# Optimization experiments

Hardware: AMD Instinct MI355X
Metric: run time of the kernel (lower is better)

## Reference

```python
import jax, jax.numpy as jnp
import numpy as np

B, S, D, H, G = 4, 2048, 1024, 16, 32
HD = D // H
LN_EPS = 1e-5


def _lin_init(key, fan_in, fan_out):
    kw, kb = jax.random.split(key)
    bound = 1.0 / np.sqrt(fan_in)
    W = jax.random.uniform(kw, (fan_in, fan_out), jnp.float32, -bound, bound)
    b = jax.random.uniform(kb, (fan_out,), jnp.float32, -bound, bound)
    return W, b


def setup_inputs() -> dict:
    key = jax.random.key(0)
    ks = jax.random.split(key, 9)
    x = jax.random.normal(ks[0], (B, S, D), jnp.float32)
    geo_features = jax.random.normal(ks[1], (B, G), jnp.float32)
    Wq, bq = _lin_init(ks[2], D, D)
    Wk, bk = _lin_init(ks[3], D, D)
    Wv, bv = _lin_init(ks[4], D, D)
    Wo, bo = _lin_init(ks[5], D, D)
    ge_W1, ge_b1 = _lin_init(ks[6], G, D)
    ln_g = jnp.ones((D,), jnp.float32)
    ln_b = jnp.zeros((D,), jnp.float32)
    ge_W2, ge_b2 = _lin_init(ks[7], D, D)
    gm_W, gm_b = _lin_init(ks[8], D, H)
    return dict(x=x, geo_features=geo_features, Wq=Wq, bq=bq, Wk=Wk, bk=bk,
                Wv=Wv, bv=bv, Wo=Wo, bo=bo, ge_W1=ge_W1, ge_b1=ge_b1,
                ln_g=ln_g, ln_b=ln_b, ge_W2=ge_W2, ge_b2=ge_b2,
                gm_W=gm_W, gm_b=gm_b)


def reference(x, geo_features, Wq, bq, Wk, bk, Wv, bv, Wo, bo,
              ge_W1, ge_b1, ln_g, ln_b, ge_W2, ge_b2, gm_W, gm_b):
    # QKV projections -> (B, H, S, HD)
    def split_heads(t):
        return t.reshape(B, S, H, HD).transpose(0, 2, 1, 3)
    Q = split_heads(x @ Wq + bq)
    K = split_heads(x @ Wk + bk)
    V = split_heads(x @ Wv + bv)

    # geo encoder: Linear -> LayerNorm -> ReLU -> Linear
    h = geo_features @ ge_W1 + ge_b1                      # (B, D)
    mu = jnp.mean(h, axis=-1, keepdims=True)
    var = jnp.mean(jnp.square(h - mu), axis=-1, keepdims=True)
    h = (h - mu) / jnp.sqrt(var + LN_EPS) * ln_g + ln_b
    h = jax.nn.relu(h)
    geo_encoded = h @ ge_W2 + ge_b2                       # (B, D)
    geo_mod = jax.nn.sigmoid(geo_encoded @ gm_W + gm_b)   # (B, H)

    scale = 1.0 / np.sqrt(HD)
    scores = jnp.einsum('bhqd,bhkd->bhqk', Q, K) * scale  # (B, H, S, S)
    scores = scores * (1.0 + geo_mod[:, :, None, None])
    attn = jax.nn.softmax(scores, axis=-1)                # dropout in eval mode: identity
    ctx = jnp.einsum('bhqk,bhkd->bhqd', attn, V)          # (B, H, S, HD)
    ctx = ctx.transpose(0, 2, 1, 3).reshape(B, S, D)
    out = ctx @ Wo + bo
    return out, attn
```

## Files before the change

### kernel.cpp

```cpp
#include <hip/hip_runtime.h>

typedef __attribute__((ext_vector_type(8))) short bf16x8;
typedef __attribute__((ext_vector_type(4))) float f32x4;
typedef __attribute__((ext_vector_type(4))) unsigned short us4;
typedef unsigned short u16;

#define MB (1024*1024)

#define WAITV(N) asm volatile("s_waitcnt vmcnt(" #N ")" ::: "memory")
#define WAITL0() asm volatile("s_waitcnt lgkmcnt(0)" ::: "memory")
#define BAR()    __builtin_amdgcn_s_barrier()
#define SCHEDB() __builtin_amdgcn_sched_barrier(0)

__device__ __forceinline__ u16 f2bf(float f) {
    unsigned u = __float_as_uint(f);
    unsigned r = (u + 0x7fffu + ((u >> 16) & 1u)) >> 16;
    return (u16)r;
}

__device__ __forceinline__ unsigned cvtpk(float a, float b) {
    unsigned r;
    asm("v_cvt_pk_bf16_f32 %0, %1, %2" : "=v"(r) : "v"(a), "v"(b));
    return r;
}

__device__ __forceinline__ f32x4 mfma16(bf16x8 a, bf16x8 b, f32x4 c) {
    return __builtin_amdgcn_mfma_f32_16x16x32_bf16(a, b, c, 0, 0, 0);
}

__device__ __forceinline__ void gload16(const void* g, void* l) {
    __builtin_amdgcn_global_load_lds(
        (__attribute__((address_space(1))) void*)(unsigned long long)g,
        (__attribute__((address_space(3))) void*)l, 16, 0, 0);
}

__global__ __launch_bounds__(256) void k_cvtx(const float* __restrict__ x, u16* __restrict__ xb) {
    const long long i = (long long)blockIdx.x * 256 + threadIdx.x;
    const float4* xp = (const float4*)x;
    float4 a = xp[i*2], b = xp[i*2+1];
    bf16x8 o;
    o[0]=(short)f2bf(a.x); o[1]=(short)f2bf(a.y); o[2]=(short)f2bf(a.z); o[3]=(short)f2bf(a.w);
    o[4]=(short)f2bf(b.x); o[5]=(short)f2bf(b.y); o[6]=(short)f2bf(b.z); o[7]=(short)f2bf(b.w);
    *(bf16x8*)&xb[i*8] = o;
}

__global__ __launch_bounds__(256) void k_wtcvt(const float* __restrict__ W0, const float* __restrict__ W1,
                                               const float* __restrict__ W2, const float* __restrict__ W3,
                                               u16* __restrict__ wt) {
    __shared__ float tl[32][33];
    const int t = threadIdx.x, z = blockIdx.z;
    const float* W = (z==0)?W0:(z==1)?W1:(z==2)?W2:W3;
    const int k0 = blockIdx.x*32, n0 = blockIdx.y*32;
    const int r = t >> 3, c4 = (t & 7) * 4;
    float4 v = *(const float4*)&W[(long long)(k0+r)*1024 + n0 + c4];
    tl[r][c4] = v.x; tl[r][c4+1] = v.y; tl[r][c4+2] = v.z; tl[r][c4+3] = v.w;
    __syncthreads();
    us4 ov;
    ov[0] = f2bf(tl[c4+0][r]); ov[1] = f2bf(tl[c4+1][r]);
    ov[2] = f2bf(tl[c4+2][r]); ov[3] = f2bf(tl[c4+3][r]);
    *(us4*)&wt[((long long)z << 20) + (long long)(n0+r)*1024 + k0 + c4] = ov;
}

__global__ __launch_bounds__(1024) void k_geo1(const float* __restrict__ geo, const float* __restrict__ W1,
                                               const float* __restrict__ b1, const float* __restrict__ lng,
                                               const float* __restrict__ lnb, float* __restrict__ hr) {
    const int b = blockIdx.x, j = threadIdx.x;
    float acc = b1[j];
    #pragma unroll 8
    for (int g = 0; g < 32; ++g) acc += geo[b*32+g] * W1[(long long)g*1024 + j];
    float s1 = acc, s2 = acc*acc;
    #pragma unroll
    for (int m = 1; m < 64; m <<= 1) { s1 += __shfl_xor(s1, m); s2 += __shfl_xor(s2, m); }
    __shared__ float r1[16], r2[16];
    __shared__ float mu_s, rv_s;
    const int wid = threadIdx.x >> 6, lid = threadIdx.x & 63;
    if (lid == 0) { r1[wid] = s1; r2[wid] = s2; }
    __syncthreads();
    if (threadIdx.x == 0) {
        float S1 = 0.f, S2 = 0.f;
        for (int i = 0; i < 16; ++i) { S1 += r1[i]; S2 += r2[i]; }
        float mu = S1 / 1024.f;
        float var = S2 / 1024.f - mu*mu;
        mu_s = mu; rv_s = rsqrtf(var + 1e-5f);
    }
    __syncthreads();
    float hv = (acc - mu_s) * rv_s * lng[j] + lnb[j];
    hr[b*1024 + j] = fmaxf(hv, 0.f);
}

__global__ __launch_bounds__(256) void k_geo2(const float* __restrict__ hr, const float* __restrict__ W2,
                                              const float* __restrict__ b2, float* __restrict__ ge) {
    const int b = blockIdx.x >> 2;
    const int j = (blockIdx.x & 3)*256 + threadIdx.x;
    __shared__ float hs[1024];
    #pragma unroll
    for (int i = 0; i < 4; ++i) hs[threadIdx.x*4 + i] = hr[b*1024 + threadIdx.x*4 + i];
    __syncthreads();
    float acc = b2[j];
    #pragma unroll 8
    for (int d = 0; d < 1024; ++d) acc += hs[d] * W2[(long long)d*1024 + j];
    ge[b*1024 + j] = acc;
}

__global__ __launch_bounds__(64) void k_geo3(const float* __restrict__ ge, const float* __restrict__ gmW,
                                             const float* __restrict__ gmb, float* __restrict__ qs) {
    const int t = threadIdx.x;
    const int b = t >> 4, hh = t & 15;
    float acc = gmb[hh];
    #pragma unroll 8
    for (int d = 0; d < 1024; ++d) acc += ge[b*1024 + d] * gmW[d*16 + hh];
    qs[t] = 0.125f * (1.f + 1.f/(1.f + __expf(-acc)));
}

__global__ __launch_bounds__(256) void k_qkv_gemm(const u16* __restrict__ xb, const u16* __restrict__ wtq,
                                                  const float* __restrict__ bq, const float* __restrict__ bk,
                                                  const float* __restrict__ bv, u16* __restrict__ outq) {
    __shared__ u16 lA[128*64];
    __shared__ u16 lB[128*64];
    const int t = threadIdx.x, z = blockIdx.z;
    const int m0 = blockIdx.y * 128, n0 = blockIdx.x * 128;
    const u16* wt = wtq + (long long)z * (1024*1024);
    const float* bias = (z==0) ? bq : (z==1) ? bk : bv;
    u16* out = outq + (long long)z * 8388608;
    const int w = t >> 6, l = t & 63, lm = l & 15, lg = l >> 4;
    const int wr = (w >> 1) * 64, wc = (w & 1) * 64;
    f32x4 acc[4][4] = {};
    const char* gA = (const char*)xb + (long long)(m0 + (t>>3))*2048 + (t&7)*16;
    const char* gB = (const char*)wt + (long long)(n0 + (t>>3))*2048 + (t&7)*16;
    char* lAp = (char*)lA + t*16;
    char* lBp = (char*)lB + t*16;
    for (int k0 = 0; k0 < 1024; k0 += 64) {
        #pragma unroll
        for (int i = 0; i < 4; ++i) {
            gload16(gA + (long long)i*32*2048, lAp + i*4096);
            gload16(gB + (long long)i*32*2048, lBp + i*4096);
        }
        gA += 128; gB += 128;
        __syncthreads();
        #pragma unroll
        for (int kk = 0; kk < 2; ++kk) {
            bf16x8 af[4], bfr[4];
            #pragma unroll
            for (int mi = 0; mi < 4; ++mi)
                af[mi] = *(const bf16x8*)((const char*)lA + (wr + mi*16 + lm)*128 + kk*64 + lg*16);
            #pragma unroll
            for (int ni = 0; ni < 4; ++ni)
                bfr[ni] = *(const bf16x8*)((const char*)lB + (wc + ni*16 + lm)*128 + kk*64 + lg*16);
            #pragma unroll
            for (int mi = 0; mi < 4; ++mi)
                #pragma unroll
                for (int ni = 0; ni < 4; ++ni)
                    acc[mi][ni] = mfma16(af[mi], bfr[ni], acc[mi][ni]);
        }
        __syncthreads();
    }
    #pragma unroll
    for (int ni = 0; ni < 4; ++ni) {
        const int n = n0 + wc + ni*16 + lm;
        const float bn = bias[n];
        const int hh = n >> 6, d = n & 63;
        #pragma unroll
        for (int mi = 0; mi < 4; ++mi) {
            #pragma unroll
            for (int r = 0; r < 4; ++r) {
                const int m = m0 + wr + mi*16 + lg*4 + r;
                const int b = m >> 11, s = m & 2047;
                out[(((long long)b*16 + hh)*2048 + s)*64 + d] = f2bf(acc[mi][ni][r] + bn);
            }
        }
    }
}

__global__ __launch_bounds__(256) void k_vtrans(const u16* __restrict__ vb, u16* __restrict__ vt) {
    __shared__ u16 tl[64][40];
    const int t = threadIdx.x;
    const int bh = blockIdx.z, s0 = blockIdx.y*64, d0 = blockIdx.x*32;
    const u16* vsrc = vb + (long long)bh*2048*64;
    {
        const int sl = t >> 2, dg = t & 3;
        bf16x8 v = *(const bf16x8*)&vsrc[(long long)(s0+sl)*64 + d0 + dg*8];
        *(bf16x8*)&tl[sl][dg*8] = v;
    }
    __syncthreads();
    {
        const int dl = t >> 3, sg = t & 7;
        bf16x8 o;
        #pragma unroll
        for (int j = 0; j < 8; ++j) o[j] = (short)tl[sg*8+j][dl];
        *(bf16x8*)&vt[((long long)bh*64 + d0+dl)*2048 + s0 + sg*8] = o;
    }
}

__global__ __launch_bounds__(512, 4) void k_attn(const u16* __restrict__ Qb, const u16* __restrict__ Kb,
                                                 const u16* __restrict__ Vt, const float* __restrict__ qsv,
                                                 float* __restrict__ attn_out, u16* __restrict__ ctxb) {
    __shared__ char lds[65536];

    const int nl = blockIdx.x;
    const int ob = (nl & 7)*64 + (nl >> 3);
    const int bh = ob >> 3, qt = ob & 7;
    const int t = threadIdx.x, w = t >> 6, l = t & 63, lm = l & 15, lg = l >> 4;
    const int q0 = qt * 256;
    const float qs = qsv[bh];

    const char* KB = (const char*)Kb + (long long)bh * 262144;
    const char* VB = (const char*)Vt + (long long)bh * 262144;

    bf16x8 qf[2][2];
    {
        const char* QB = (const char*)Qb + (long long)bh * 262144;
        #pragma unroll
        for (int ms = 0; ms < 2; ++ms)
            #pragma unroll
            for (int kc = 0; kc < 2; ++kc)
                qf[ms][kc] = *(const bf16x8*)(QB + (long long)(q0 + w*32 + ms*16 + lm)*128 + kc*64 + lg*16);
    }

    const int off = t*16;
    const int row = off >> 7, cb = off & 127;
    const int offA = off;
    const int srcK = row*128  + (cb ^ ((row & 7) << 4));
    const int srcV = row*4096 + (cb ^ ((row & 7) << 4));

    float lsum[2] = {0.f, 0.f};
    {
        gload16(KB + srcK, lds + offA);
        gload16(KB + 8192 + srcK, lds + 8192 + offA);
        SCHEDB();
        WAITV(1); BAR(); SCHEDB();

        int cb_ = 0, sb_ = 2;
        for (int kt = 0; kt < 32; ++kt) {
            const int ktn = (kt < 30) ? kt + 2 : 31;
            gload16(KB + (long long)ktn*8192 + srcK, lds + sb_*8192 + offA);
            SCHEDB();
            const char* kb = lds + cb_*8192;
            #pragma unroll
            for (int ns = 0; ns < 4; ++ns) {
                const int rowb = ns*16 + lm;
                const int tag = (rowb & 7) << 4;
                bf16x8 kf0 = *(const bf16x8*)(kb + rowb*128 + ((lg*16) ^ tag));
                bf16x8 kf1 = *(const bf16x8*)(kb + rowb*128 + ((64 + lg*16) ^ tag));
                #pragma unroll
                for (int ms = 0; ms < 2; ++ms) {
                    f32x4 a = {};
                    a = mfma16(kf0, qf[ms][0], a);
                    a = mfma16(kf1, qf[ms][1], a);
                    lsum[ms] += __expf(a[0]*qs) + __expf(a[1]*qs)
                              + __expf(a[2]*qs) + __expf(a[3]*qs);
                }
            }
            WAITV(1); BAR(); SCHEDB();
            cb_ = (cb_ == 2) ? 0 : cb_ + 1;
            sb_ = (sb_ == 2) ? 0 : sb_ + 1;
        }
    }
    WAITV(0); BAR(); SCHEDB();

    float invl[2];
    #pragma unroll
    for (int ms = 0; ms < 2; ++ms) {
        float v = lsum[ms];
        v += __shfl_xor(v, 16);
        v += __shfl_xor(v, 32);
        invl[ms] = 1.f / v;
    }

    char* lP = lds + 32768;
    float* aL = attn_out + ((long long)bh*2048 + q0 + w*32 + lm)*2048 + lg*4;
    f32x4 cacc[2][4] = {};

    {
        gload16(KB + srcK, lds + offA);
        gload16(VB + srcV, lds + 16384 + offA);
        SCHEDB();
        WAITV(0); BAR(); SCHEDB();

        for (int kt = 0; kt < 32; ++kt) {
            const int cur = kt & 1, nxt = cur ^ 1;
            const int ktn = (kt < 31) ? kt + 1 : 31;
            gload16(KB + (long long)ktn*8192 + srcK, lds + nxt*8192 + offA);
            gload16(VB + (long long)ktn*128 + srcV, lds + 16384 + nxt*8192 + offA);
            SCHEDB();

            const char* kb = lds + cur*8192;
            #pragma unroll
            for (int ns = 0; ns < 4; ++ns) {
                const int rowb = ns*16 + lm;
                const int tag = (rowb & 7) << 4;
                bf16x8 kf0 = *(const bf16x8*)(kb + rowb*128 + ((lg*16) ^ tag));
                bf16x8 kf1 = *(const bf16x8*)(kb + rowb*128 + ((64 + lg*16) ^ tag));
                #pragma unroll
                for (int ms = 0; ms < 2; ++ms) {
                    f32x4 a = {};
                    a = mfma16(kf0, qf[ms][0], a);
                    a = mfma16(kf1, qf[ms][1], a);
                    const float p0 = __expf(a[0]*qs) * invl[ms];
                    const float p1 = __expf(a[1]*qs) * invl[ms];
                    const float p2 = __expf(a[2]*qs) * invl[ms];
                    const float p3 = __expf(a[3]*qs) * invl[ms];
                    f32x4 pv4 = {p0, p1, p2, p3};
                    __builtin_nontemporal_store(pv4, (f32x4*)(aL + ms*32768 + kt*64 + ns*16));
                    const int prow = w*32 + ms*16 + lm;
                    const int ptag = (prow & 7) << 4;
                    uint2 pk; pk.x = cvtpk(p0, p1); pk.y = cvtpk(p2, p3);
                    *(uint2*)(lP + prow*128 + ((32*ns + 8*lg) ^ ptag)) = pk;
                }
            }
            WAITL0(); SCHEDB();

            const char* vb = lds + 16384 + cur*8192;
            #pragma unroll
            for (int ks = 0; ks < 2; ++ks) {
                bf16x8 pa[2];
                #pragma unroll
                for (int ms = 0; ms < 2; ++ms) {
                    const int prow = w*32 + ms*16 + lm;
                    pa[ms] = *(const bf16x8*)(lP + prow*128 + ((ks*64 + lg*16) ^ ((prow & 7) << 4)));
                }
                #pragma unroll
                for (int dn = 0; dn < 4; ++dn) {
                    const int rv = dn*16 + lm;
                    bf16x8 vf = *(const bf16x8*)(vb + rv*128 + ((ks*64 + lg*16) ^ ((rv & 7) << 4)));
                    cacc[0][dn] = mfma16(pa[0], vf, cacc[0][dn]);
                    cacc[1][dn] = mfma16(pa[1], vf, cacc[1][dn]);
                }
            }
            WAITV(8); BAR(); SCHEDB();
        }
    }

    const int b = bh >> 4, hh = bh & 15;
    #pragma unroll
    for (int ms = 0; ms < 2; ++ms)
        #pragma unroll
        for (int dn = 0; dn < 4; ++dn)
            #pragma unroll
            for (int r = 0; r < 4; ++r) {
                const int q = q0 + w*32 + ms*16 + lg*4 + r;
                ctxb[(((long long)b*2048 + q)*16 + hh)*64 + dn*16 + lm] = f2bf(cacc[ms][dn][r]);
            }
}

__global__ __launch_bounds__(256) void k_o_gemm(const u16* __restrict__ ab, const u16* __restrict__ wt,
                                                const float* __restrict__ bo, float* __restrict__ outf) {
    __shared__ u16 lA[128*64];
    __shared__ u16 lB[128*64];
    const int t = threadIdx.x;
    const int m0 = blockIdx.y * 128, n0 = blockIdx.x * 128;
    const int w = t >> 6, l = t & 63, lm = l & 15, lg = l >> 4;
    const int wr = (w >> 1) * 64, wc = (w & 1) * 64;
    f32x4 acc[4][4] = {};
    const char* gA = (const char*)ab + (long long)(m0 + (t>>3))*2048 + (t&7)*16;
    const char* gB = (const char*)wt + (long long)(n0 + (t>>3))*2048 + (t&7)*16;
    char* lAp = (char*)lA + t*16;
    char* lBp = (char*)lB + t*16;
    for (int k0 = 0; k0 < 1024; k0 += 64) {
        #pragma unroll
        for (int i = 0; i < 4; ++i) {
            gload16(gA + (long long)i*32*2048, lAp + i*4096);
            gload16(gB + (long long)i*32*2048, lBp + i*4096);
        }
        gA += 128; gB += 128;
        __syncthreads();
        #pragma unroll
        for (int kk = 0; kk < 2; ++kk) {
            bf16x8 af[4], bfr[4];
            #pragma unroll
            for (int mi = 0; mi < 4; ++mi)
                af[mi] = *(const bf16x8*)((const char*)lA + (wr + mi*16 + lm)*128 + kk*64 + lg*16);
            #pragma unroll
            for (int ni = 0; ni < 4; ++ni)
                bfr[ni] = *(const bf16x8*)((const char*)lB + (wc + ni*16 + lm)*128 + kk*64 + lg*16);
            #pragma unroll
            for (int mi = 0; mi < 4; ++mi)
                #pragma unroll
                for (int ni = 0; ni < 4; ++ni)
                    acc[mi][ni] = mfma16(af[mi], bfr[ni], acc[mi][ni]);
        }
        __syncthreads();
    }
    #pragma unroll
    for (int ni = 0; ni < 4; ++ni) {
        const int n = n0 + wc + ni*16 + lm;
        const float bn = bo[n];
        #pragma unroll
        for (int mi = 0; mi < 4; ++mi) {
            #pragma unroll
            for (int r = 0; r < 4; ++r) {
                const int m = m0 + wr + mi*16 + lg*4 + r;
                outf[(long long)m*1024 + n] = acc[mi][ni][r] + bn;
            }
        }
    }
}

extern "C" void kernel_launch(void* const* d_in, const int* in_sizes, int n_in,
                              void* d_out, int out_size, void* d_ws, size_t ws_size,
                              hipStream_t stream) {
    const float* x    = (const float*)d_in[0];
    const float* geo  = (const float*)d_in[1];
    const float* Wq   = (const float*)d_in[2];
    const float* bq   = (const float*)d_in[3];
    const float* Wk   = (const float*)d_in[4];
    const float* bk   = (const float*)d_in[5];
    const float* Wv   = (const float*)d_in[6];
    const float* bv   = (const float*)d_in[7];
    const float* Wo   = (const float*)d_in[8];
    const float* bo   = (const float*)d_in[9];
    const float* geW1 = (const float*)d_in[10];
    const float* geb1 = (const float*)d_in[11];
    const float* lng  = (const float*)d_in[12];
    const float* lnb  = (const float*)d_in[13];
    const float* geW2 = (const float*)d_in[14];
    const float* geb2 = (const float*)d_in[15];
    const float* gmW  = (const float*)d_in[16];
    const float* gmb  = (const float*)d_in[17];

    char* ws = (char*)d_ws;
    u16* xb   = (u16*)(ws + 0);
    u16* wt   = (u16*)(ws + 16*(size_t)MB);
    u16* qkv  = (u16*)(ws + 24*(size_t)MB);
    u16* Qb   = qkv;
    u16* Kb   = (u16*)(ws + 40*(size_t)MB);
    u16* Vb   = (u16*)(ws + 56*(size_t)MB);
    u16* Vt   = (u16*)(ws + 72*(size_t)MB);
    u16* ctx  = Vb;
    float* hr = (float*)(ws + 88*(size_t)MB);
    float* ge = (float*)(ws + 88*(size_t)MB + 65536);
    float* qsb= (float*)(ws + 88*(size_t)MB + 131072);

    float* outf = (float*)d_out;
    float* attn = outf + 8388608;

    hipLaunchKernelGGL(k_cvtx,    dim3(4096),      dim3(256),  0, stream, x, xb);
    hipLaunchKernelGGL(k_wtcvt,   dim3(32,32,4),   dim3(256),  0, stream, Wq, Wk, Wv, Wo, wt);
    hipLaunchKernelGGL(k_geo1,    dim3(4),         dim3(1024), 0, stream, geo, geW1, geb1, lng, lnb, hr);
    hipLaunchKernelGGL(k_geo2,    dim3(16),        dim3(256),  0, stream, hr, geW2, geb2, ge);
    hipLaunchKernelGGL(k_geo3,    dim3(1),         dim3(64),   0, stream, ge, gmW, gmb, qsb);
    hipLaunchKernelGGL(k_qkv_gemm,dim3(8,64,3),    dim3(256),  0, stream, xb, wt, bq, bk, bv, qkv);
    hipLaunchKernelGGL(k_vtrans,  dim3(2,32,64),   dim3(256),  0, stream, Vb, Vt);
    hipLaunchKernelGGL(k_attn,    dim3(512),       dim3(512),  0, stream, Qb, Kb, Vt, qsb, attn, ctx);
    hipLaunchKernelGGL(k_o_gemm,  dim3(8,64),      dim3(256),  0, stream, ctx, wt + 3*1048576, bo, outf);
}
```

Baseline: 583.1 us.

## Fuse geo encoder kernels, vectorize GEMM epilogues, use cached attn stores

Merges the three geo-encoder kernels into one 4-block kernel that keeps intermediates in shared memory and computes the head projection with a partial-sum reduction, removing two launches. The QKV and output GEMMs swap MFMA operand order so each lane holds four contiguous columns, which allows packed bf16x4 and float4 stores with vectorized bias loads in place of scalar stores. The attention-probability write changes from a nontemporal store to a regular store. The geo kernel now runs its 1024x1024 GEMV with only 4 blocks, so it has less parallelism than the previous 16-block version.

Result: slower. 595.9 us (+2.2%).

```diff
diff --git a/kernel.cpp b/kernel.cpp
--- a/kernel.cpp
+++ b/kernel.cpp
@@ -61,22 +61,28 @@
     *(us4*)&wt[((long long)z << 20) + (long long)(n0+r)*1024 + k0 + c4] = ov;
 }
 
-__global__ __launch_bounds__(1024) void k_geo1(const float* __restrict__ geo, const float* __restrict__ W1,
-                                               const float* __restrict__ b1, const float* __restrict__ lng,
-                                               const float* __restrict__ lnb, float* __restrict__ hr) {
+__global__ __launch_bounds__(1024) void k_geo(const float* __restrict__ geo, const float* __restrict__ W1,
+                                              const float* __restrict__ b1, const float* __restrict__ lng,
+                                              const float* __restrict__ lnb, const float* __restrict__ W2,
+                                              const float* __restrict__ b2, const float* __restrict__ gmW,
+                                              const float* __restrict__ gmb, float* __restrict__ qs) {
     const int b = blockIdx.x, j = threadIdx.x;
+    __shared__ float hs[1024];
+    __shared__ float ges[1024];
+    __shared__ float parts[64][16];
+    __shared__ float r1[16], r2[16];
+    __shared__ float mu_s, rv_s;
+
     float acc = b1[j];
     #pragma unroll 8
     for (int g = 0; g < 32; ++g) acc += geo[b*32+g] * W1[(long long)g*1024 + j];
     float s1 = acc, s2 = acc*acc;
     #pragma unroll
     for (int m = 1; m < 64; m <<= 1) { s1 += __shfl_xor(s1, m); s2 += __shfl_xor(s2, m); }
-    __shared__ float r1[16], r2[16];
-    __shared__ float mu_s, rv_s;
-    const int wid = threadIdx.x >> 6, lid = threadIdx.x & 63;
+    const int wid = j >> 6, lid = j & 63;
     if (lid == 0) { r1[wid] = s1; r2[wid] = s2; }
     __syncthreads();
-    if (threadIdx.x == 0) {
+    if (j == 0) {
         float S1 = 0.f, S2 = 0.f;
         for (int i = 0; i < 16; ++i) { S1 += r1[i]; S2 += r2[i]; }
         float mu = S1 / 1024.f;
@@ -85,31 +91,29 @@
     }
     __syncthreads();
     float hv = (acc - mu_s) * rv_s * lng[j] + lnb[j];
-    hr[b*1024 + j] = fmaxf(hv, 0.f);
-}
-
-__global__ __launch_bounds__(256) void k_geo2(const float* __restrict__ hr, const float* __restrict__ W2,
-                                              const float* __restrict__ b2, float* __restrict__ ge) {
-    const int b = blockIdx.x >> 2;
-    const int j = (blockIdx.x & 3)*256 + threadIdx.x;
-    __shared__ float hs[1024];
-    #pragma unroll
-    for (int i = 0; i < 4; ++i) hs[threadIdx.x*4 + i] = hr[b*1024 + threadIdx.x*4 + i];
-    __syncthreads();
-    float acc = b2[j];
+    hs[j] = fmaxf(hv, 0.f);
+    __syncthreads();
+
+    float acc2 = b2[j];
     #pragma unroll 8
-    for (int d = 0; d < 1024; ++d) acc += hs[d] * W2[(long long)d*1024 + j];
-    ge[b*1024 + j] = acc;
-}
-
-__global__ __launch_bounds__(64) void k_geo3(const float* __restrict__ ge, const float* __restrict__ gmW,
-                                             const float* __restrict__ gmb, float* __restrict__ qs) {
-    const int t = threadIdx.x;
-    const int b = t >> 4, hh = t & 15;
-    float acc = gmb[hh];
-    #pragma unroll 8
-    for (int d = 0; d < 1024; ++d) acc += ge[b*1024 + d] * gmW[d*16 + hh];
-    qs[t] = 0.125f * (1.f + 1.f/(1.f + __expf(-acc)));
+    for (int d = 0; d < 1024; ++d) acc2 += hs[d] * W2[(long long)d*1024 + j];
+    ges[j] = acc2;
+    __syncthreads();
+
+    const int hh = j & 15, seg = j >> 4;
+    float part = 0.f;
+    #pragma unroll
+    for (int dd = 0; dd < 16; ++dd) {
+        const int d = seg*16 + dd;
+        part += ges[d] * gmW[d*16 + hh];
+    }
+    parts[seg][hh] = part;
+    __syncthreads();
+    if (j < 16) {
+        float s = gmb[j];
+        for (int k = 0; k < 64; ++k) s += parts[k][j];
+        qs[b*16 + j] = 0.125f * (1.f + 1.f/(1.f + __expf(-s)));
+    }
 }
 
 __global__ __launch_bounds__(256) void k_qkv_gemm(const u16* __restrict__ xb, const u16* __restrict__ wtq,
@@ -150,23 +154,23 @@
             for (int mi = 0; mi < 4; ++mi)
                 #pragma unroll
                 for (int ni = 0; ni < 4; ++ni)
-                    acc[mi][ni] = mfma16(af[mi], bfr[ni], acc[mi][ni]);
+                    acc[mi][ni] = mfma16(bfr[ni], af[mi], acc[mi][ni]);
         }
         __syncthreads();
     }
     #pragma unroll
-    for (int ni = 0; ni < 4; ++ni) {
-        const int n = n0 + wc + ni*16 + lm;
-        const float bn = bias[n];
-        const int hh = n >> 6, d = n & 63;
-        #pragma unroll
-        for (int mi = 0; mi < 4; ++mi) {
-            #pragma unroll
-            for (int r = 0; r < 4; ++r) {
-                const int m = m0 + wr + mi*16 + lg*4 + r;
-                const int b = m >> 11, s = m & 2047;
-                out[(((long long)b*16 + hh)*2048 + s)*64 + d] = f2bf(acc[mi][ni][r] + bn);
-            }
+    for (int mi = 0; mi < 4; ++mi) {
+        const int m = m0 + wr + mi*16 + lm;
+        const int b = m >> 11, s = m & 2047;
+        #pragma unroll
+        for (int ni = 0; ni < 4; ++ni) {
+            const int nb = n0 + wc + ni*16 + lg*4;
+            const float4 bn4 = *(const float4*)&bias[nb];
+            const int hh = nb >> 6, d = nb & 63;
+            uint2 pk;
+            pk.x = cvtpk(acc[mi][ni][0] + bn4.x, acc[mi][ni][1] + bn4.y);
+            pk.y = cvtpk(acc[mi][ni][2] + bn4.z, acc[mi][ni][3] + bn4.w);
+            *(uint2*)&out[(((long long)b*16 + hh)*2048 + s)*64 + d] = pk;
         }
     }
 }
@@ -300,7 +304,7 @@
                     const float p2 = __expf(a[2]*qs) * invl[ms];
                     const float p3 = __expf(a[3]*qs) * invl[ms];
                     f32x4 pv4 = {p0, p1, p2, p3};
-                    __builtin_nontemporal_store(pv4, (f32x4*)(aL + ms*32768 + kt*64 + ns*16));
+                    *(f32x4*)(aL + ms*32768 + kt*64 + ns*16) = pv4;
                     const int prow = w*32 + ms*16 + lm;
                     const int ptag = (prow & 7) << 4;
                     uint2 pk; pk.x = cvtpk(p0, p1); pk.y = cvtpk(p2, p3);
@@ -376,21 +380,20 @@
             for (int mi = 0; mi < 4; ++mi)
                 #pragma unroll
                 for (int ni = 0; ni < 4; ++ni)
-                    acc[mi][ni] = mfma16(af[mi], bfr[ni], acc[mi][ni]);
+                    acc[mi][ni] = mfma16(bfr[ni], af[mi], acc[mi][ni]);
         }
         __syncthreads();
     }
     #pragma unroll
-    for (int ni = 0; ni < 4; ++ni) {
-        const int n = n0 + wc + ni*16 + lm;
-        const float bn = bo[n];
-        #pragma unroll
-        for (int mi = 0; mi < 4; ++mi) {
-            #pragma unroll
-            for (int r = 0; r < 4; ++r) {
-                const int m = m0 + wr + mi*16 + lg*4 + r;
-                outf[(long long)m*1024 + n] = acc[mi][ni][r] + bn;
-            }
+    for (int mi = 0; mi < 4; ++mi) {
+        const int m = m0 + wr + mi*16 + lm;
+        #pragma unroll
+        for (int ni = 0; ni < 4; ++ni) {
+            const int nb = n0 + wc + ni*16 + lg*4;
+            const float4 bn4 = *(const float4*)&bo[nb];
+            f32x4 v = acc[mi][ni];
+            v[0] += bn4.x; v[1] += bn4.y; v[2] += bn4.z; v[3] += bn4.w;
+            *(f32x4*)&outf[(long long)m*1024 + nb] = v;
         }
     }
 }
@@ -426,18 +429,14 @@
     u16* Vb   = (u16*)(ws + 56*(size_t)MB);
     u16* Vt   = (u16*)(ws + 72*(size_t)MB);
     u16* ctx  = Vb;
-    float* hr = (float*)(ws + 88*(size_t)MB);
-    float* ge = (float*)(ws + 88*(size_t)MB + 65536);
-    float* qsb= (float*)(ws + 88*(size_t)MB + 131072);
+    float* qsb= (float*)(ws + 88*(size_t)MB);
 
     float* outf = (float*)d_out;
     float* attn = outf + 8388608;
 
     hipLaunchKernelGGL(k_cvtx,    dim3(4096),      dim3(256),  0, stream, x, xb);
     hipLaunchKernelGGL(k_wtcvt,   dim3(32,32,4),   dim3(256),  0, stream, Wq, Wk, Wv, Wo, wt);
-    hipLaunchKernelGGL(k_geo1,    dim3(4),         dim3(1024), 0, stream, geo, geW1, geb1, lng, lnb, hr);
-    hipLaunchKernelGGL(k_geo2,    dim3(16),        dim3(256),  0, stream, hr, geW2, geb2, ge);
-    hipLaunchKernelGGL(k_geo3,    dim3(1),         dim3(64),   0, stream, ge, gmW, gmb, qsb);
+    hipLaunchKernelGGL(k_geo,     dim3(4),         dim3(1024), 0, stream, geo, geW1, geb1, lng, lnb, geW2, geb2, gmW, gmb, qsb);
     hipLaunchKernelGGL(k_qkv_gemm,dim3(8,64,3),    dim3(256),  0, stream, xb, wt, bq, bk, bv, qkv);
     hipLaunchKernelGGL(k_vtrans,  dim3(2,32,64),   dim3(256),  0, stream, Vb, Vt);
     hipLaunchKernelGGL(k_attn,    dim3(512),       dim3(512),  0, stream, Qb, Kb, Vt, qsb, attn, ctx);
```
